# Optimization experiments

Measured on AMD Instinct MI355X. Metric: run time of the kernel, lower is better.

Reference implementation:

```python
import jax, jax.numpy as jnp
import numpy as np
import math


def _alibi_slopes(num_heads: int) -> np.ndarray:
    def power_of_2(n):
        ratio = 2.0 ** (-8.0 / n)
        return np.array([ratio ** i for i in range(n)], dtype=np.float32)
    if math.log2(num_heads).is_integer():
        return power_of_2(num_heads)
    nearest = 2 ** math.floor(math.log2(num_heads))
    return np.concatenate([power_of_2(nearest), power_of_2(2 * nearest)[::2][: num_heads - nearest]])


def _rmsnorm(x, w, eps=1e-6):
    var = jnp.mean(x * x, axis=-1, keepdims=True)
    return x * jax.lax.rsqrt(var + eps) * w


def setup_inputs() -> dict:
    key = jax.random.key(0)
    ks = jax.random.split(key, 6)
    B, S, M = 2, 2048, 1024
    H, KV, D = 16, 4, 64
    s = 0.02
    return {
        "features": jax.random.normal(ks[0], (B, S, M), jnp.float32),
        "wq": jax.random.normal(ks[1], (H * D, M), jnp.float32) * s,
        "wk": jax.random.normal(ks[2], (KV * D, M), jnp.float32) * s,
        "wv": jax.random.normal(ks[3], (KV * D, M), jnp.float32) * s,
        "wo": jax.random.normal(ks[4], (M, H * D), jnp.float32) * s,
        "q_norm_w": jnp.ones((H * D,), jnp.float32),
        "k_norm_w": jnp.ones((KV * D,), jnp.float32),
        "num_heads": 16,
        "num_kv_heads": 4,
        "head_dim": 64,
        "sliding_window": 512,
    }


def reference(features, wq, wk, wv, wo, q_norm_w, k_norm_w, num_heads, num_kv_heads, head_dim, sliding_window):
    B, S, M = features.shape
    H, KV, D = num_heads, num_kv_heads, head_dim
    kv_rep = H // KV

    q = features @ wq.T                                   # [B,S,H*D]
    k = features @ wk.T                                   # [B,S,KV*D]
    v = features @ wv.T                                   # [B,S,KV*D]
    q = _rmsnorm(q, q_norm_w)
    k = _rmsnorm(k, k_norm_w)

    q = q.reshape(B, S, H, D).transpose(0, 2, 1, 3)       # [B,H,S,D]
    k = k.reshape(B, S, KV, D)
    v = v.reshape(B, S, KV, D)
    k = jnp.repeat(k, kv_rep, axis=2).transpose(0, 2, 1, 3)  # [B,H,S,D]
    v = jnp.repeat(v, kv_rep, axis=2).transpose(0, 2, 1, 3)

    pos = jnp.arange(S)
    rel = pos[None, :] - pos[:, None]                     # [S,S], j - i
    slopes = jnp.asarray(_alibi_slopes(H))
    bias = slopes[:, None, None] * rel.astype(features.dtype)  # [H,S,S]
    invalid = (rel > 0) | (rel < -sliding_window)         # causal + left window
    bias = jnp.where(invalid[None], -jnp.inf, bias)

    scores = jnp.einsum("bhqd,bhkd->bhqk", q, k) / math.sqrt(D)
    attn = jax.nn.softmax(scores + bias[None], axis=-1)
    out = jnp.einsum("bhqk,bhkd->bhqd", attn, v)
    out = out.transpose(0, 2, 1, 3).reshape(B, S, H * D)
    return out @ wo.T
```

## Files before the change

kernel.cpp:

```cpp
#include <hip/hip_runtime.h>
#include <hip/hip_bf16.h>

typedef __bf16 bf16_t;
typedef bf16_t bf16x8 __attribute__((ext_vector_type(8)));
typedef bf16_t bf16x4 __attribute__((ext_vector_type(4)));
typedef float  f32x4  __attribute__((ext_vector_type(4)));
typedef float  f32x16 __attribute__((ext_vector_type(16)));

__device__ __forceinline__ f32x4 mfma16(bf16x8 a, bf16x8 b, f32x4 c) {
  return __builtin_amdgcn_mfma_f32_16x16x32_bf16(a, b, c, 0, 0, 0);
}
__device__ __forceinline__ f32x16 mfma32(bf16x8 a, bf16x8 b, f32x16 c) {
  return __builtin_amdgcn_mfma_f32_32x32x16_bf16(a, b, c, 0, 0, 0);
}

__global__ __launch_bounds__(256) void cast_all_k(const float* __restrict__ f,
                                                  const float* __restrict__ wq,
                                                  const float* __restrict__ wk,
                                                  const float* __restrict__ wv,
                                                  const float* __restrict__ wo,
                                                  bf16_t* __restrict__ Xbf,
                                                  bf16_t* __restrict__ Wqkv,
                                                  bf16_t* __restrict__ Wo) {
  int i = blockIdx.x * 256 + threadIdx.x;
  const float* src; bf16_t* dst; int off;
  if (i < 1048576)      { src = f;  dst = Xbf;                 off = 0; }
  else if (i < 1310720) { src = wq; dst = Wqkv;                off = 1048576; }
  else if (i < 1376256) { src = wk; dst = Wqkv + 1024 * 1024;  off = 1310720; }
  else if (i < 1441792) { src = wv; dst = Wqkv + 1280 * 1024;  off = 1376256; }
  else if (i < 1703936) { src = wo; dst = Wo;                  off = 1441792; }
  else return;
  int j = i - off;
  float4 v = reinterpret_cast<const float4*>(src)[j];
  bf16x4 o = { (bf16_t)v.x, (bf16_t)v.y, (bf16_t)v.z, (bf16_t)v.w };
  reinterpret_cast<bf16x4*>(dst)[j] = o;
}

__global__ __launch_bounds__(256) void gemm_bt(const bf16_t* __restrict__ A,
                                               const bf16_t* __restrict__ B,
                                               float* __restrict__ C,
                                               int M, int N, int K) {
  __shared__ __align__(16) unsigned short sA[2][128 * 64];
  __shared__ __align__(16) unsigned short sB[2][128 * 64];
  const int tid = threadIdx.x;
  const int lane = tid & 63;
  const int wid = tid >> 6;
  const int wm = wid >> 1, wn = wid & 1;
  const int lr = lane & 15, lg = lane >> 4;
  const int m0 = blockIdx.y * 128, n0 = blockIdx.x * 128;

  f32x4 acc[4][4] = {};

  auto STAGE = [&](int buf, int k0) {
#pragma unroll
    for (int r = 0; r < 4; ++r) {
      int e = r * 2048 + tid * 8;
      int row = e >> 6;
      int c = ((e >> 3) & 7) ^ (row & 7);
      const bf16_t* ga = A + (size_t)(m0 + row) * K + k0 + c * 8;
      __builtin_amdgcn_global_load_lds(
          (const __attribute__((address_space(1))) void*)ga,
          (__attribute__((address_space(3))) void*)(&sA[buf][r * 2048 + wid * 512]), 16, 0, 0);
      const bf16_t* gb = B + (size_t)(n0 + row) * K + k0 + c * 8;
      __builtin_amdgcn_global_load_lds(
          (const __attribute__((address_space(1))) void*)gb,
          (__attribute__((address_space(3))) void*)(&sB[buf][r * 2048 + wid * 512]), 16, 0, 0);
    }
  };

  const int nt = K >> 6;
  STAGE(0, 0);
  __syncthreads();
  int cur = 0;
  for (int t = 0; t < nt; ++t) {
    if (t + 1 < nt) STAGE(cur ^ 1, (t + 1) << 6);
#pragma unroll
    for (int ks = 0; ks < 2; ++ks) {
      bf16x8 afr[4], bfr[4];
#pragma unroll
      for (int m = 0; m < 4; ++m) {
        int row = wm * 64 + m * 16 + lr;
        int sc = (ks * 4 + lg) ^ (row & 7);
        afr[m] = *reinterpret_cast<const bf16x8*>(&sA[cur][row * 64 + sc * 8]);
      }
#pragma unroll
      for (int n = 0; n < 4; ++n) {
        int row = wn * 64 + n * 16 + lr;
        int sc = (ks * 4 + lg) ^ (row & 7);
        bfr[n] = *reinterpret_cast<const bf16x8*>(&sB[cur][row * 64 + sc * 8]);
      }
#pragma unroll
      for (int m = 0; m < 4; ++m)
#pragma unroll
        for (int n = 0; n < 4; ++n)
          acc[m][n] = mfma16(afr[m], bfr[n], acc[m][n]);
    }
    __syncthreads();
    cur ^= 1;
  }
#pragma unroll
  for (int m = 0; m < 4; ++m)
#pragma unroll
    for (int n = 0; n < 4; ++n) {
      int row = m0 + wm * 64 + m * 16 + lg * 4;
      int col = n0 + wn * 64 + n * 16 + lr;
#pragma unroll
      for (int r2 = 0; r2 < 4; ++r2)
        C[(size_t)(row + r2) * N + col] = acc[m][n][r2];
    }
}

__global__ __launch_bounds__(256) void rmsnorm_k(const float* __restrict__ qkv,
                                                 const float* __restrict__ qw,
                                                 const float* __restrict__ kw,
                                                 bf16_t* __restrict__ qn,
                                                 bf16_t* __restrict__ kn) {
  const int row = blockIdx.x;
  const int b = row >> 11, s = row & 2047;
  const int tid = threadIdx.x;
  const float* rp = qkv + (size_t)row * 1536;
  float4 q4 = *reinterpret_cast<const float4*>(rp + tid * 4);
  float kv1 = rp[1024 + tid];
  float sq = q4.x * q4.x + q4.y * q4.y + q4.z * q4.z + q4.w * q4.w;
  float sk = kv1 * kv1;
#pragma unroll
  for (int d = 1; d < 64; d <<= 1) {
    sq += __shfl_xor(sq, d, 64);
    sk += __shfl_xor(sk, d, 64);
  }
  __shared__ float red[2][4];
  if ((tid & 63) == 0) { red[0][tid >> 6] = sq; red[1][tid >> 6] = sk; }
  __syncthreads();
  sq = red[0][0] + red[0][1] + red[0][2] + red[0][3];
  sk = red[1][0] + red[1][1] + red[1][2] + red[1][3];
  const float rq = rsqrtf(sq * (1.0f / 1024.0f) + 1e-6f);
  const float rk = rsqrtf(sk * (1.0f / 256.0f) + 1e-6f);
  float4 w4 = *reinterpret_cast<const float4*>(qw + tid * 4);
  const int c = tid * 4, hh = c >> 6, d0 = c & 63;
  bf16x4 o = { (bf16_t)(q4.x * rq * w4.x), (bf16_t)(q4.y * rq * w4.y),
               (bf16_t)(q4.z * rq * w4.z), (bf16_t)(q4.w * rq * w4.w) };
  *reinterpret_cast<bf16x4*>(qn + ((size_t)((b * 16 + hh) * 2048 + s)) * 64 + d0) = o;
  const int kvh = tid >> 6, dk = tid & 63;
  kn[((size_t)((b * 4 + kvh) * 2048 + s)) * 64 + dk] = (bf16_t)(kv1 * rk * kw[tid]);
}

__global__ __launch_bounds__(256) void transpose_v_k(const float* __restrict__ qkv,
                                                     bf16_t* __restrict__ vt) {
  __shared__ float t[64][65];
  const int s0 = blockIdx.x * 64;
  const int b = blockIdx.y >> 2, kv = blockIdx.y & 3;
  const int tid = threadIdx.x;
  const int r = tid >> 2, cg = (tid & 3) * 16;
  const float* src = qkv + (size_t)(b * 2048 + s0 + r) * 1536 + 1280 + kv * 64 + cg;
#pragma unroll
  for (int j = 0; j < 4; ++j) {
    float4 v = *reinterpret_cast<const float4*>(src + j * 4);
    t[r][cg + j * 4 + 0] = v.x; t[r][cg + j * 4 + 1] = v.y;
    t[r][cg + j * 4 + 2] = v.z; t[r][cg + j * 4 + 3] = v.w;
  }
  __syncthreads();
  const int dl = tid >> 4;
  const int sl = (tid & 15) * 4;
#pragma unroll
  for (int p = 0; p < 4; ++p) {
    const int d = dl + p * 16;
    bf16x4 o = { (bf16_t)t[sl + 0][d], (bf16_t)t[sl + 1][d],
                 (bf16_t)t[sl + 2][d], (bf16_t)t[sl + 3][d] };
    *reinterpret_cast<bf16x4*>(vt + ((size_t)((b * 4 + kv) * 64 + d)) * 2048 + s0 + sl) = o;
  }
}

__global__ __launch_bounds__(256, 4) void attn_k(const bf16_t* __restrict__ qn,
                                                 const bf16_t* __restrict__ kn,
                                                 const bf16_t* __restrict__ vt,
                                                 bf16_t* __restrict__ ao) {
  constexpr int S = 2048, D = 64, H = 16, KV = 4, WIN = 512;
  const int wid = threadIdx.x >> 6;
  const int pair = wid >> 1;
  const int kh = wid & 1;
  const int qblk = blockIdx.x * 2 + pair;
  const int h = blockIdx.y, b = blockIdx.z;
  const int kv = h >> 2;
  const int lane = threadIdx.x & 63;
  const int c = lane & 31;
  const int hi = lane >> 5;
  const int qbase = qblk * 32;
  const int q = qbase + c;

  __shared__ float mls[2][2][2][32];
  __shared__ float accbuf[2][64][33];

  const bf16_t* qp = qn + ((size_t)(b * H + h) * S + q) * D + hi * 8;
  bf16x8 qf[4];
#pragma unroll
  for (int cd = 0; cd < 4; ++cd) qf[cd] = *reinterpret_cast<const bf16x8*>(qp + cd * 16);

  const bf16_t* kb = kn + (size_t)(b * KV + kv) * S * D;
  const bf16_t* vb = vt + (size_t)(b * KV + kv) * D * S;

  const float L2E = 1.4426950408889634f;
  const float c1 = L2E / 8.0f;
  const float c2 = exp2f(-0.5f * (float)h) * L2E;

  f32x16 acc0 = {}, acc1 = {};
  float m_run = -3.0e38f, l_run = 0.0f;

  const int ktTop = qbase >> 5;
  const int kt0 = (qbase >= WIN) ? ((qbase - WIN) >> 5) : 0;

  for (int kt = ktTop - kh; kt >= kt0; kt -= 2) {
    const int k0 = kt << 5;
    const bf16_t* kp = kb + (size_t)(k0 + c) * D + hi * 8;
    f32x16 sfa = {};
#pragma unroll
    for (int cd = 0; cd < 4; ++cd) {
      bf16x8 kf = *reinterpret_cast<const bf16x8*>(kp + cd * 16);
      sfa = mfma32(kf, qf[cd], sfa);
    }
    const bool mtop = (kt == ktTop);
    const bool mbot = (k0 + WIN < qbase + 32);
    float t[16];
    float pmax = -3.0e38f;
    if (mtop | mbot) {
#pragma unroll
      for (int r = 0; r < 16; ++r) {
        const int kk = k0 + (r & 3) + 8 * (r >> 2) + 4 * hi;
        const int rel = kk - q;
        float tv = sfa[r] * c1 + c2 * (float)rel;
        if (rel > 0 || rel < -WIN) tv = -3.0e38f;
        t[r] = tv;
        pmax = fmaxf(pmax, tv);
      }
    } else {
      const float bb = c2 * (float)(k0 + 4 * hi - q);
#pragma unroll
      for (int r = 0; r < 16; ++r) {
        const float koff = (float)((r & 3) + 8 * (r >> 2));
        float tv = fmaf(sfa[r], c1, fmaf(koff, c2, bb));
        t[r] = tv;
        pmax = fmaxf(pmax, tv);
      }
    }
    pmax = fmaxf(pmax, __shfl_xor(pmax, 32, 64));
    if (!__all(pmax <= m_run + 8.0f)) {
      const float mnew = fmaxf(m_run, pmax);
      const float sc = exp2f(m_run - mnew);
      m_run = mnew;
      l_run *= sc;
#pragma unroll
      for (int r = 0; r < 16; ++r) {
        const int qi = (r & 3) + 8 * (r >> 2) + 4 * hi;
        const float scr = __shfl(sc, qi, 64);
        acc0[r] *= scr;
        acc1[r] *= scr;
      }
    }
    float rs = 0.0f;
    unsigned w[8];
#pragma unroll
    for (int i = 0; i < 8; ++i) {
      float e0 = exp2f(t[2 * i] - m_run);
      float e1 = exp2f(t[2 * i + 1] - m_run);
      rs += e0 + e1;
      union { bf16_t hh[2]; unsigned u; } pk;
      pk.hh[0] = (bf16_t)e0; pk.hh[1] = (bf16_t)e1;
      w[i] = pk.u;
    }
    rs += __shfl_xor(rs, 32, 64);
    l_run += rs;
    unsigned s0 = __shfl_xor(w[0], 32, 64), s1 = __shfl_xor(w[1], 32, 64);
    unsigned s2 = __shfl_xor(w[2], 32, 64), s3 = __shfl_xor(w[3], 32, 64);
    unsigned s4 = __shfl_xor(w[4], 32, 64), s5 = __shfl_xor(w[5], 32, 64);
    unsigned s6 = __shfl_xor(w[6], 32, 64), s7 = __shfl_xor(w[7], 32, 64);
    union { unsigned u[4]; bf16x8 v; } pa0, pa1;
    if (hi == 0) {
      pa0.u[0] = w[0]; pa0.u[1] = w[1]; pa0.u[2] = s0; pa0.u[3] = s1;
      pa1.u[0] = w[4]; pa1.u[1] = w[5]; pa1.u[2] = s4; pa1.u[3] = s5;
    } else {
      pa0.u[0] = s2; pa0.u[1] = s3; pa0.u[2] = w[2]; pa0.u[3] = w[3];
      pa1.u[0] = s6; pa1.u[1] = s7; pa1.u[2] = w[6]; pa1.u[3] = w[7];
    }
    const bf16_t* vp = vb + (size_t)c * S + k0 + hi * 8;
    bf16x8 v00 = *reinterpret_cast<const bf16x8*>(vp);
    bf16x8 v01 = *reinterpret_cast<const bf16x8*>(vp + 16);
    bf16x8 v10 = *reinterpret_cast<const bf16x8*>(vp + 32 * S);
    bf16x8 v11 = *reinterpret_cast<const bf16x8*>(vp + 32 * S + 16);
    acc0 = mfma32(pa0.v, v00, acc0);
    acc0 = mfma32(pa1.v, v01, acc0);
    acc1 = mfma32(pa0.v, v10, acc1);
    acc1 = mfma32(pa1.v, v11, acc1);
  }

  mls[pair][kh][0][c] = m_run;
  mls[pair][kh][1][c] = l_run;
  __syncthreads();
  const float mo = mls[pair][kh ^ 1][0][c];
  const float lo = mls[pair][kh ^ 1][1][c];
  const float mt = fmaxf(m_run, mo);
  const float sc_self = exp2f(m_run - mt);
#pragma unroll
  for (int r = 0; r < 16; ++r) {
    const int qi = (r & 3) + 8 * (r >> 2) + 4 * hi;
    const float scr = __shfl(sc_self, qi, 64);
    acc0[r] *= scr;
    acc1[r] *= scr;
  }
  if (kh == 1) {
#pragma unroll
    for (int r = 0; r < 16; ++r) {
      accbuf[pair][lane][r] = acc0[r];
      accbuf[pair][lane][r + 16] = acc1[r];
    }
  }
  __syncthreads();
  if (kh == 0) {
    const float l_tot = l_run * sc_self + lo * exp2f(mo - mt);
#pragma unroll
    for (int r = 0; r < 16; ++r) {
      acc0[r] += accbuf[pair][lane][r];
      acc1[r] += accbuf[pair][lane][r + 16];
    }
#pragma unroll
    for (int r = 0; r < 16; ++r) {
      const int qi = (r & 3) + 8 * (r >> 2) + 4 * hi;
      const float lr = __shfl(l_tot, qi, 64);
      const float inv = 1.0f / lr;
      bf16_t* op = ao + ((size_t)(b * S + qbase + qi)) * 1024 + h * 64 + c;
      op[0]  = (bf16_t)(acc0[r] * inv);
      op[32] = (bf16_t)(acc1[r] * inv);
    }
  }
}

extern "C" void kernel_launch(void* const* d_in, const int* in_sizes, int n_in,
                              void* d_out, int out_size, void* d_ws, size_t ws_size,
                              hipStream_t stream) {
  const float* features = (const float*)d_in[0];
  const float* wq = (const float*)d_in[1];
  const float* wk = (const float*)d_in[2];
  const float* wv = (const float*)d_in[3];
  const float* wo = (const float*)d_in[4];
  const float* qw = (const float*)d_in[5];
  const float* kw = (const float*)d_in[6];
  float* out = (float*)d_out;

  bf16_t* Xbf  = (bf16_t*)d_ws;
  bf16_t* Wqkv = Xbf + 4096 * 1024;
  bf16_t* Wo   = Wqkv + 1536 * 1024;
  float*  QKVr = (float*)(Wo + 1024 * 1024);
  bf16_t* Qn   = (bf16_t*)(QKVr + 4096 * 1536);
  bf16_t* Kn   = Qn + 2 * 16 * 2048 * 64;
  bf16_t* Vt   = Kn + 2 * 4 * 2048 * 64;
  bf16_t* Ao   = Vt + 2 * 4 * 64 * 2048;

  cast_all_k<<<6656, 256, 0, stream>>>(features, wq, wk, wv, wo, Xbf, Wqkv, Wo);
  gemm_bt<<<dim3(12, 32), 256, 0, stream>>>(Xbf, Wqkv, QKVr, 4096, 1536, 1024);
  rmsnorm_k<<<4096, 256, 0, stream>>>(QKVr, qw, kw, Qn, Kn);
  transpose_v_k<<<dim3(32, 8), 256, 0, stream>>>(QKVr, Vt);
  attn_k<<<dim3(32, 16, 2), 256, 0, stream>>>(Qn, Kn, Vt, Ao);
  gemm_bt<<<dim3(8, 32), 256, 0, stream>>>(Ao, Wo, out, 4096, 1024, 1024);
}
```

Measured before the change: 104.0 us.

## Tile V layout per key block, prefetch K, reorder attention grid by KV head

The V transpose now writes V in per-32-key tiles (d×32 contiguous), so each attention iteration reads V from one contiguous 4KB block instead of rows strided by sequence length. The attention loop prefetches the next K fragment and issues V loads before the QK MFMAs to hide global latency. The grid is reordered so blocks sharing a KV head and batch are adjacent, which should improve L2 reuse. Scores are recomputed in the exp pass instead of stored in a t[] array to cut register use, and the launch bound minimum-occupancy hint is dropped, at the risk of more registers and lower occupancy.

```diff
diff --git a/kernel.cpp b/kernel.cpp
--- a/kernel.cpp
+++ b/kernel.cpp
@@ -148,7 +148,8 @@
                                                      bf16_t* __restrict__ vt) {
   __shared__ float t[64][65];
   const int s0 = blockIdx.x * 64;
-  const int b = blockIdx.y >> 2, kv = blockIdx.y & 3;
+  const int bkv = blockIdx.y;
+  const int b = bkv >> 2, kv = bkv & 3;
   const int tid = threadIdx.x;
   const int r = tid >> 2, cg = (tid & 3) * 16;
   const float* src = qkv + (size_t)(b * 2048 + s0 + r) * 1536 + 1280 + kv * 64 + cg;
@@ -161,26 +162,29 @@
   __syncthreads();
   const int dl = tid >> 4;
   const int sl = (tid & 15) * 4;
+  const int kt = (s0 >> 5) + (sl >> 5);
+  const int kk = sl & 31;
 #pragma unroll
   for (int p = 0; p < 4; ++p) {
     const int d = dl + p * 16;
     bf16x4 o = { (bf16_t)t[sl + 0][d], (bf16_t)t[sl + 1][d],
                  (bf16_t)t[sl + 2][d], (bf16_t)t[sl + 3][d] };
-    *reinterpret_cast<bf16x4*>(vt + ((size_t)((b * 4 + kv) * 64 + d)) * 2048 + s0 + sl) = o;
-  }
-}
-
-__global__ __launch_bounds__(256, 4) void attn_k(const bf16_t* __restrict__ qn,
-                                                 const bf16_t* __restrict__ kn,
-                                                 const bf16_t* __restrict__ vt,
-                                                 bf16_t* __restrict__ ao) {
+    *reinterpret_cast<bf16x4*>(vt + (size_t)bkv * 131072 + (size_t)kt * 2048 + d * 32 + kk) = o;
+  }
+}
+
+__global__ __launch_bounds__(256) void attn_k(const bf16_t* __restrict__ qn,
+                                              const bf16_t* __restrict__ kn,
+                                              const bf16_t* __restrict__ vt,
+                                              bf16_t* __restrict__ ao) {
   constexpr int S = 2048, D = 64, H = 16, KV = 4, WIN = 512;
+  const int bkv = blockIdx.x;
+  const int b = bkv >> 2, kv = bkv & 3;
+  const int h = kv * 4 + blockIdx.z;
   const int wid = threadIdx.x >> 6;
   const int pair = wid >> 1;
   const int kh = wid & 1;
-  const int qblk = blockIdx.x * 2 + pair;
-  const int h = blockIdx.y, b = blockIdx.z;
-  const int kv = h >> 2;
+  const int qblk = blockIdx.y * 2 + pair;
   const int lane = threadIdx.x & 63;
   const int c = lane & 31;
   const int hi = lane >> 5;
@@ -195,8 +199,8 @@
 #pragma unroll
   for (int cd = 0; cd < 4; ++cd) qf[cd] = *reinterpret_cast<const bf16x8*>(qp + cd * 16);
 
-  const bf16_t* kb = kn + (size_t)(b * KV + kv) * S * D;
-  const bf16_t* vb = vt + (size_t)(b * KV + kv) * D * S;
+  const bf16_t* kb = kn + (size_t)bkv * S * D;
+  const bf16_t* vb = vt + (size_t)bkv * 131072;
 
   const float L2E = 1.4426950408889634f;
   const float c1 = L2E / 8.0f;
@@ -208,38 +212,53 @@
   const int ktTop = qbase >> 5;
   const int kt0 = (qbase >= WIN) ? ((qbase - WIN) >> 5) : 0;
 
-  for (int kt = ktTop - kh; kt >= kt0; kt -= 2) {
+  struct Kfrag { bf16x8 v[4]; };
+  auto loadK = [&](int kt) {
+    Kfrag f;
+    const bf16_t* kp = kb + (((size_t)(kt << 5) + c) << 6) + hi * 8;
+    f.v[0] = *reinterpret_cast<const bf16x8*>(kp);
+    f.v[1] = *reinterpret_cast<const bf16x8*>(kp + 16);
+    f.v[2] = *reinterpret_cast<const bf16x8*>(kp + 32);
+    f.v[3] = *reinterpret_cast<const bf16x8*>(kp + 48);
+    return f;
+  };
+
+  const int ktstart = ktTop - kh;
+  Kfrag kcur;
+  if (ktstart >= kt0) kcur = loadK(ktstart);
+
+  for (int kt = ktstart; kt >= kt0; kt -= 2) {
+    const bool haveNext = (kt - 2 >= kt0);
+    Kfrag knx;
+    if (haveNext) knx = loadK(kt - 2);
+    const bf16_t* vp = vb + ((size_t)kt << 11) + c * 32 + hi * 8;
+    bf16x8 v00 = *reinterpret_cast<const bf16x8*>(vp);
+    bf16x8 v01 = *reinterpret_cast<const bf16x8*>(vp + 16);
+    bf16x8 v10 = *reinterpret_cast<const bf16x8*>(vp + 1024);
+    bf16x8 v11 = *reinterpret_cast<const bf16x8*>(vp + 1024 + 16);
+
     const int k0 = kt << 5;
-    const bf16_t* kp = kb + (size_t)(k0 + c) * D + hi * 8;
     f32x16 sfa = {};
-#pragma unroll
-    for (int cd = 0; cd < 4; ++cd) {
-      bf16x8 kf = *reinterpret_cast<const bf16x8*>(kp + cd * 16);
-      sfa = mfma32(kf, qf[cd], sfa);
-    }
-    const bool mtop = (kt == ktTop);
-    const bool mbot = (k0 + WIN < qbase + 32);
-    float t[16];
+    sfa = mfma32(kcur.v[0], qf[0], sfa);
+    sfa = mfma32(kcur.v[1], qf[1], sfa);
+    sfa = mfma32(kcur.v[2], qf[2], sfa);
+    sfa = mfma32(kcur.v[3], qf[3], sfa);
+
+    const bool edge = (kt == ktTop) | (k0 + WIN < qbase + 32);
     float pmax = -3.0e38f;
-    if (mtop | mbot) {
+    const float bb = c2 * (float)(k0 + 4 * hi - q);
+    if (edge) {
 #pragma unroll
       for (int r = 0; r < 16; ++r) {
-        const int kk = k0 + (r & 3) + 8 * (r >> 2) + 4 * hi;
-        const int rel = kk - q;
+        const int rel = k0 + (r & 3) + 8 * (r >> 2) + 4 * hi - q;
         float tv = sfa[r] * c1 + c2 * (float)rel;
-        if (rel > 0 || rel < -WIN) tv = -3.0e38f;
-        t[r] = tv;
+        tv = (rel > 0 || rel < -WIN) ? -3.0e38f : tv;
         pmax = fmaxf(pmax, tv);
       }
     } else {
-      const float bb = c2 * (float)(k0 + 4 * hi - q);
-#pragma unroll
-      for (int r = 0; r < 16; ++r) {
-        const float koff = (float)((r & 3) + 8 * (r >> 2));
-        float tv = fmaf(sfa[r], c1, fmaf(koff, c2, bb));
-        t[r] = tv;
-        pmax = fmaxf(pmax, tv);
-      }
+#pragma unroll
+      for (int r = 0; r < 16; ++r)
+        pmax = fmaxf(pmax, fmaf(sfa[r], c1, fmaf((float)((r & 3) + 8 * (r >> 2)), c2, bb)));
     }
     pmax = fmaxf(pmax, __shfl_xor(pmax, 32, 64));
     if (!__all(pmax <= m_run + 8.0f)) {
@@ -257,14 +276,38 @@
     }
     float rs = 0.0f;
     unsigned w[8];
-#pragma unroll
-    for (int i = 0; i < 8; ++i) {
-      float e0 = exp2f(t[2 * i] - m_run);
-      float e1 = exp2f(t[2 * i + 1] - m_run);
-      rs += e0 + e1;
-      union { bf16_t hh[2]; unsigned u; } pk;
-      pk.hh[0] = (bf16_t)e0; pk.hh[1] = (bf16_t)e1;
-      w[i] = pk.u;
+    if (edge) {
+#pragma unroll
+      for (int i = 0; i < 8; ++i) {
+        float e2[2];
+#pragma unroll
+        for (int j = 0; j < 2; ++j) {
+          const int r = 2 * i + j;
+          const int rel = k0 + (r & 3) + 8 * (r >> 2) + 4 * hi - q;
+          float tv = sfa[r] * c1 + c2 * (float)rel;
+          tv = (rel > 0 || rel < -WIN) ? -3.0e38f : tv;
+          e2[j] = exp2f(tv - m_run);
+        }
+        rs += e2[0] + e2[1];
+        union { bf16_t hh[2]; unsigned u; } pk;
+        pk.hh[0] = (bf16_t)e2[0]; pk.hh[1] = (bf16_t)e2[1];
+        w[i] = pk.u;
+      }
+    } else {
+#pragma unroll
+      for (int i = 0; i < 8; ++i) {
+        float e2[2];
+#pragma unroll
+        for (int j = 0; j < 2; ++j) {
+          const int r = 2 * i + j;
+          float tv = fmaf(sfa[r], c1, fmaf((float)((r & 3) + 8 * (r >> 2)), c2, bb));
+          e2[j] = exp2f(tv - m_run);
+        }
+        rs += e2[0] + e2[1];
+        union { bf16_t hh[2]; unsigned u; } pk;
+        pk.hh[0] = (bf16_t)e2[0]; pk.hh[1] = (bf16_t)e2[1];
+        w[i] = pk.u;
+      }
     }
     rs += __shfl_xor(rs, 32, 64);
     l_run += rs;
@@ -280,15 +323,11 @@
       pa0.u[0] = s2; pa0.u[1] = s3; pa0.u[2] = w[2]; pa0.u[3] = w[3];
       pa1.u[0] = s6; pa1.u[1] = s7; pa1.u[2] = w[6]; pa1.u[3] = w[7];
     }
-    const bf16_t* vp = vb + (size_t)c * S + k0 + hi * 8;
-    bf16x8 v00 = *reinterpret_cast<const bf16x8*>(vp);
-    bf16x8 v01 = *reinterpret_cast<const bf16x8*>(vp + 16);
-    bf16x8 v10 = *reinterpret_cast<const bf16x8*>(vp + 32 * S);
-    bf16x8 v11 = *reinterpret_cast<const bf16x8*>(vp + 32 * S + 16);
     acc0 = mfma32(pa0.v, v00, acc0);
     acc0 = mfma32(pa1.v, v01, acc0);
     acc1 = mfma32(pa0.v, v10, acc1);
     acc1 = mfma32(pa1.v, v11, acc1);
+    if (haveNext) kcur = knx;
   }
 
   mls[pair][kh][0][c] = m_run;
@@ -357,6 +396,6 @@
   gemm_bt<<<dim3(12, 32), 256, 0, stream>>>(Xbf, Wqkv, QKVr, 4096, 1536, 1024);
   rmsnorm_k<<<4096, 256, 0, stream>>>(QKVr, qw, kw, Qn, Kn);
   transpose_v_k<<<dim3(32, 8), 256, 0, stream>>>(QKVr, Vt);
-  attn_k<<<dim3(32, 16, 2), 256, 0, stream>>>(Qn, Kn, Vt, Ao);
+  attn_k<<<dim3(8, 32, 4), 256, 0, stream>>>(Qn, Kn, Vt, Ao);
   gemm_bt<<<dim3(8, 32), 256, 0, stream>>>(Ao, Wo, out, 4096, 1024, 1024);
 }
```

Result: slower. 121.0 us (+16.3%).
